# Performance work log

Hardware: AMD Instinct MI355X
Metric: run time of the kernel (lower is better)

The kernel has to match this reference:

```python
import jax, jax.numpy as jnp
import numpy as np

B, T, D, H, DFF = 2, 2048, 1024, 16, 4096
DK = D // H
EPS = 1e-12
NEG = -1e9

def _ln(x, g, b):
    m = jnp.mean(x, axis=-1, keepdims=True)
    v = jnp.mean((x - m) ** 2, axis=-1, keepdims=True)
    return (x - m) / jnp.sqrt(v + EPS) * g + b

def setup_inputs() -> dict:
    key = jax.random.key(0)
    ks = jax.random.split(key, 8)
    s = 0.02
    return {
        "x": jax.random.normal(ks[0], (B, T, D), jnp.float32),
        "mask": jnp.ones((1, 1, T, T), jnp.int32),
        "wq": jax.random.normal(ks[1], (D, D), jnp.float32) * s,
        "bq": jnp.zeros((D,), jnp.float32),
        "wk": jax.random.normal(ks[2], (D, D), jnp.float32) * s,
        "bk": jnp.zeros((D,), jnp.float32),
        "wv": jax.random.normal(ks[3], (D, D), jnp.float32) * s,
        "bv": jnp.zeros((D,), jnp.float32),
        "wo": jax.random.normal(ks[4], (D, D), jnp.float32) * s,
        "bo": jnp.zeros((D,), jnp.float32),
        "w1": jax.random.normal(ks[5], (DFF, D), jnp.float32) * s,
        "b1": jnp.zeros((DFF,), jnp.float32),
        "w2": jax.random.normal(ks[6], (D, DFF), jnp.float32) * s,
        "b2": jnp.zeros((D,), jnp.float32),
        "g1": jnp.ones((D,), jnp.float32),
        "beta1": jnp.zeros((D,), jnp.float32),
        "g2": jnp.ones((D,), jnp.float32),
        "beta2": jnp.zeros((D,), jnp.float32),
    }

def reference(x, mask, wq, bq, wk, bk, wv, bv, wo, bo, w1, b1, w2, b2, g1, beta1, g2, beta2):
    # pre-norm (note: residual taken from ln1 output, faithful to source)
    xn = _ln(x, g1, beta1)
    # torch Linear: y = x @ W.T + b
    def proj(w, b):
        return (jnp.einsum('btd,ed->bte', xn, w) + b).reshape(B, T, H, DK).transpose(0, 2, 1, 3)
    q = proj(wq, bq)  # [B,H,T,DK]
    k = proj(wk, bk)
    v = proj(wv, bv)
    scores = jnp.einsum('bhqd,bhkd->bhqk', q, k) / jnp.sqrt(jnp.float32(DK))
    scores = jnp.where(mask == 0, jnp.float32(NEG), scores)
    weights = jax.nn.softmax(scores, axis=-1)  # dropout is identity in eval
    att = jnp.einsum('bhqk,bhkd->bhqd', weights, v)
    att = att.transpose(0, 2, 1, 3).reshape(B, T, D)
    h = jnp.einsum('btd,ed->bte', att, wo) + bo
    x = xn + h
    x = _ln(x, g2, beta2)
    ff = jax.nn.relu(jnp.einsum('btd,fd->btf', x, w1) + b1)
    ff = jnp.einsum('btf,df->btd', ff, w2) + b2
    return x + ff
```

## Files before the change

### kernel.cpp

```cpp
#include <hip/hip_runtime.h>

typedef unsigned short u16;
typedef __attribute__((ext_vector_type(8))) short short8;
typedef __attribute__((ext_vector_type(4))) float f32x4;
typedef __attribute__((ext_vector_type(4))) unsigned short u16x4;
typedef __attribute__((ext_vector_type(2))) unsigned int u32x2;

#define DEV static __device__ __forceinline__

DEV u16 f2b(float f) {
    unsigned int u = __builtin_bit_cast(unsigned int, f);
    u += 0x7FFFu + ((u >> 16) & 1u);
    return (u16)(u >> 16);
}
DEV float b2f(u16 v) {
    unsigned int u = ((unsigned int)v) << 16;
    return __builtin_bit_cast(float, u);
}
DEV void gload16(const void* g, void* l) {
    __builtin_amdgcn_global_load_lds((const __attribute__((address_space(1))) void*)g,
                                     (__attribute__((address_space(3))) void*)l,
                                     16, 0, 0);
}
DEV unsigned int cvt_pk(float lo, float hi) {
    unsigned int r;
    asm("v_cvt_pk_bf16_f32 %0, %1, %2" : "=v"(r) : "v"(lo), "v"(hi));
    return r;
}

static constexpr float KSCALE = 0.18033688011112042f;

__global__ __launch_bounds__(256) void cvt_all_k(
    const float* __restrict__ wq, const float* __restrict__ wk,
    const float* __restrict__ wv, const float* __restrict__ wo,
    const float* __restrict__ w1, const float* __restrict__ w2,
    u16* __restrict__ wqkv, u16* __restrict__ wo_b,
    u16* __restrict__ w1_b, u16* __restrict__ w2_b) {
    int bid = blockIdx.x;
    const float* s; u16* d; int off;
    if (bid < 1024)      { s = wq; d = wqkv;              off = bid; }
    else if (bid < 2048) { s = wk; d = wqkv + 1024*1024;  off = bid - 1024; }
    else if (bid < 3072) { s = wv; d = wqkv + 2048*1024;  off = bid - 2048; }
    else if (bid < 4096) { s = wo; d = wo_b;              off = bid - 3072; }
    else if (bid < 8192) { s = w1; d = w1_b;              off = bid - 4096; }
    else                 { s = w2; d = w2_b;              off = bid - 8192; }
    int i = off * 256 + threadIdx.x;
    float4 v = ((const float4*)s)[i];
    u16x4 o;
    o[0] = f2b(v.x); o[1] = f2b(v.y); o[2] = f2b(v.z); o[3] = f2b(v.w);
    ((u16x4*)d)[i] = o;
}

template <int INTYPE>
__global__ __launch_bounds__(256) void ln_k(const void* __restrict__ in,
                                            const float* __restrict__ g,
                                            const float* __restrict__ be,
                                            u16* __restrict__ outb) {
    int row = blockIdx.x;
    int t = threadIdx.x;
    float v[4];
    if constexpr (INTYPE == 0) {
        float4 x = ((const float4*)((const float*)in + (size_t)row * 1024))[t];
        v[0] = x.x; v[1] = x.y; v[2] = x.z; v[3] = x.w;
    } else {
        u16x4 x = ((const u16x4*)((const u16*)in + (size_t)row * 1024))[t];
#pragma unroll
        for (int i = 0; i < 4; i++) v[i] = b2f(x[i]);
    }
    float s = v[0] + v[1] + v[2] + v[3];
    float s2 = v[0] * v[0] + v[1] * v[1] + v[2] * v[2] + v[3] * v[3];
#pragma unroll
    for (int off = 1; off < 64; off <<= 1) {
        s += __shfl_xor(s, off);
        s2 += __shfl_xor(s2, off);
    }
    __shared__ float red[8];
    int wid = t >> 6, lane = t & 63;
    if (lane == 0) { red[wid] = s; red[4 + wid] = s2; }
    __syncthreads();
    float S = red[0] + red[1] + red[2] + red[3];
    float S2 = red[4] + red[5] + red[6] + red[7];
    float mean = S * (1.f / 1024.f);
    float var = fmaxf(S2 * (1.f / 1024.f) - mean * mean, 0.f);
    float rinv = rsqrtf(var + 1e-12f);
    float4 gv = ((const float4*)g)[t];
    float4 bv = ((const float4*)be)[t];
    u16x4 o;
    o[0] = f2b((v[0] - mean) * rinv * gv.x + bv.x);
    o[1] = f2b((v[1] - mean) * rinv * gv.y + bv.y);
    o[2] = f2b((v[2] - mean) * rinv * gv.z + bv.z);
    o[3] = f2b((v[3] - mean) * rinv * gv.w + bv.w);
    ((u16x4*)(outb + (size_t)row * 1024))[t] = o;
}

template <int EPI>
__global__ __launch_bounds__(512, 2) void gemm256(
    const u16* __restrict__ A, const u16* __restrict__ Bw,
    const float* __restrict__ b0, const float* __restrict__ b1,
    const float* __restrict__ b2, u16* __restrict__ outb,
    u16* __restrict__ vt, int M, int N, int K) {
    __shared__ u16 SB[3 * 16384];
    int tid = threadIdx.x, wid = tid >> 6, lane = tid & 63;
    int l15 = lane & 15, l4 = lane >> 4;
    int m0 = blockIdx.y * 256, n0 = blockIdx.x * 256;
    int wr = wid >> 2, wc = wid & 3;

    f32x4 acc[8][4] = {};

    int srow = tid >> 2;
    int sc = (tid & 3) * 8;
    const u16* Ag  = A  + (size_t)(m0 + srow) * K + sc;
    const u16* Ag2 = Ag + (size_t)128 * K;
    const u16* Bg  = Bw + (size_t)(n0 + srow) * K + sc;
    const u16* Bg2 = Bg + (size_t)128 * K;
    int ldst = wid * 1024;

    auto stageA = [&](int t, int bufi) {
        char* base = (char*)SB + bufi * 32768;
        size_t ko = (size_t)t * 32;
        gload16(Ag + ko, base + ldst);
        gload16(Ag2 + ko, base + 8192 + ldst);
    };
    auto stageB = [&](int t, int bufi) {
        char* base = (char*)SB + bufi * 32768 + 16384;
        size_t ko = (size_t)t * 32;
        gload16(Bg + ko, base + ldst);
        gload16(Bg2 + ko, base + 8192 + ldst);
    };

    const int NT = K >> 5;
    stageA(0, 0); stageB(0, 0);
    stageA(1, 1); stageB(1, 1);

    int cb = 0;
    for (int i = 0; i < NT; ++i) {
        if (i == NT - 1) asm volatile("s_waitcnt vmcnt(0)" ::: "memory");
        else             asm volatile("s_waitcnt vmcnt(4)" ::: "memory");
        __builtin_amdgcn_s_barrier();
        __builtin_amdgcn_sched_barrier(0);
        int sb = cb + 2; if (sb >= 3) sb -= 3;

        const u16* Abuf = SB + cb * 16384;
        const u16* Bbuf = Abuf + 8192;
        const u16* ap = &Abuf[(wr * 128 + l15) * 32 + l4 * 8];
        const u16* bp = &Bbuf[(wc * 64 + l15) * 32 + l4 * 8];
        short8 af[8], bfr[4];
#pragma unroll
        for (int x = 0; x < 4; x++) {
            af[x]  = *(const short8*)(ap + x * 512);
            bfr[x] = *(const short8*)(bp + x * 512);
        }
        if (i + 2 < NT) stageA(i + 2, sb);
#pragma unroll
        for (int x = 4; x < 8; x++) af[x] = *(const short8*)(ap + x * 512);
        if (i + 2 < NT) stageB(i + 2, sb);
        __builtin_amdgcn_s_setprio(1);
#pragma unroll
        for (int mi = 0; mi < 8; mi++)
#pragma unroll
            for (int ni = 0; ni < 4; ni++)
                acc[mi][ni] = __builtin_amdgcn_mfma_f32_16x16x32_bf16(
                    af[mi], bfr[ni], acc[mi][ni], 0, 0, 0);
        __builtin_amdgcn_s_setprio(0);
        cb = (cb == 2) ? 0 : cb + 1;
    }

#pragma unroll
    for (int mi = 0; mi < 8; mi++) {
#pragma unroll
        for (int ni = 0; ni < 4; ni++) {
            int n = n0 + wc * 64 + ni * 16 + l15;
            int mr = m0 + wr * 128 + mi * 16 + l4 * 4;
            if constexpr (EPI == 0) {
                if (n0 < 2048) {
                    float bias = (n < 1024) ? b0[n] : b1[n - 1024];
                    float scale = (n < 1024) ? 1.f : KSCALE;
#pragma unroll
                    for (int r = 0; r < 4; r++)
                        outb[(size_t)(mr + r) * 2048 + n] =
                            f2b((acc[mi][ni][r] + bias) * scale);
                } else {
                    float bias = b2[n - 2048];
                    int bidx = m0 >> 11;
                    int tb = mr & 2047;
                    u16x4 pk;
#pragma unroll
                    for (int r = 0; r < 4; r++) pk[r] = f2b(acc[mi][ni][r] + bias);
                    *(u16x4*)&vt[((size_t)(bidx * 1024 + (n - 2048))) * 2048 + tb] = pk;
                }
            } else {
                float bias = b0[n];
#pragma unroll
                for (int r = 0; r < 4; r++)
                    outb[(size_t)(mr + r) * N + n] =
                        f2b(fmaxf(acc[mi][ni][r] + bias, 0.f));
            }
        }
    }
}

template <int EPI, int BM>
__global__ __launch_bounds__(256) void gemm_bt(
    const u16* __restrict__ A, const u16* __restrict__ Bw,
    const float* __restrict__ b0, u16* __restrict__ outb,
    float* __restrict__ outf, const u16* __restrict__ res,
    int M, int N, int K) {
    constexpr int MFR = BM / 32;
    constexpr int BS = (BM + 128) * 32;
    __shared__ u16 SB[3 * BS];
    int tid = threadIdx.x, wid = tid >> 6, lane = tid & 63;
    int l15 = lane & 15, l4 = lane >> 4;
    int m0 = blockIdx.y * BM, n0 = blockIdx.x * 128;
    int wr = wid >> 1, wc = wid & 1;

    f32x4 acc[MFR][4] = {};

    int srow = tid >> 2;
    int scol = (tid & 3) * 8;
    const u16* Ag  = A  + (size_t)(m0 + srow) * K + scol;
    const u16* Ag2 = Ag + (size_t)64 * K;
    const u16* Bg  = Bw + (size_t)(n0 + srow) * K + scol;
    const u16* Bg2 = Bg + (size_t)64 * K;
    int ldst = wid * 1024;

    auto stage = [&](int t, int bufi) {
        char* base = (char*)SB + (size_t)bufi * (BS * 2);
        size_t ko = (size_t)t * 32;
        gload16(Ag + ko, base + ldst);
        if constexpr (BM == 128) gload16(Ag2 + ko, base + 4096 + ldst);
        gload16(Bg + ko, base + BM * 64 + ldst);
        gload16(Bg2 + ko, base + BM * 64 + 4096 + ldst);
    };

    const int NT = K >> 5;
    stage(0, 0);
    stage(1, 1);

    int cb = 0;
    for (int i = 0; i < NT; ++i) {
        if (i == NT - 1) {
            asm volatile("s_waitcnt vmcnt(0)" ::: "memory");
        } else if constexpr (BM == 128) {
            asm volatile("s_waitcnt vmcnt(4)" ::: "memory");
        } else {
            asm volatile("s_waitcnt vmcnt(3)" ::: "memory");
        }
        __builtin_amdgcn_s_barrier();
        __builtin_amdgcn_sched_barrier(0);
        int sb = cb + 2; if (sb >= 3) sb -= 3;
        if (i + 2 < NT) stage(i + 2, sb);

        const u16* Abuf = SB + (size_t)cb * BS;
        const u16* Bbuf = Abuf + BM * 32;
        short8 af[MFR], bfr[4];
        const u16* ap = &Abuf[(wr * (BM / 2) + l15) * 32 + l4 * 8];
        const u16* bp = &Bbuf[(wc * 64 + l15) * 32 + l4 * 8];
#pragma unroll
        for (int i2 = 0; i2 < MFR; i2++) af[i2] = *(const short8*)(ap + i2 * 512);
#pragma unroll
        for (int i2 = 0; i2 < 4; i2++) bfr[i2] = *(const short8*)(bp + i2 * 512);
#pragma unroll
        for (int mi = 0; mi < MFR; mi++)
#pragma unroll
            for (int ni = 0; ni < 4; ni++)
                acc[mi][ni] = __builtin_amdgcn_mfma_f32_16x16x32_bf16(
                    af[mi], bfr[ni], acc[mi][ni], 0, 0, 0);
        cb = (cb == 2) ? 0 : cb + 1;
    }

    int mbase = m0 + wr * (BM / 2);
    int nbase = n0 + wc * 64;
#pragma unroll
    for (int mi = 0; mi < MFR; mi++) {
#pragma unroll
        for (int ni = 0; ni < 4; ni++) {
            int n = nbase + ni * 16 + l15;
            int mr = mbase + mi * 16 + l4 * 4;
            float bias = b0[n];
            if constexpr (EPI == 1) {
#pragma unroll
                for (int i = 0; i < 4; i++) {
                    size_t off = (size_t)(mr + i) * N + n;
                    outb[off] = f2b(acc[mi][ni][i] + bias + b2f(res[off]));
                }
            } else {
#pragma unroll
                for (int i = 0; i < 4; i++) {
                    size_t off = (size_t)(mr + i) * N + n;
                    outf[off] = acc[mi][ni][i] + bias + b2f(res[off]);
                }
            }
        }
    }
}

#define ATT_STAGE(KN, VN, TILE) do {                                          \
    size_t koff_ = (size_t)(TILE) * 64 * 2048;                                \
    gload16(Kg + koff_, (char*)(KN) + ldst);                                  \
    gload16(Kg + koff_ + 32 * 2048, (char*)(KN) + 4096 + ldst);               \
    gload16(Vg + (TILE) * 64, (char*)(VN) + ldst);                            \
    gload16(Vg + (TILE) * 64 + 32 * 2048, (char*)(VN) + 4096 + ldst);         \
} while (0)

#define ATT_BODY(KL, VL, PRE, WAITSTR) do {                                   \
    PRE;                                                                      \
    asm volatile("s_waitcnt " WAITSTR ::: "memory");                          \
    __builtin_amdgcn_s_barrier();                                             \
    __builtin_amdgcn_sched_barrier(0);                                        \
    f32x4 s_acc[4][2] = {};                                                   \
    _Pragma("unroll")                                                         \
    for (int kvt = 0; kvt < 4; kvt++) {                                       \
        int row = kvt * 16 + l15;                                             \
        short8 kf0 = *(const short8*)&(KL)[row * 64 + ((l4) ^ (row & 7)) * 8]; \
        short8 kf1 = *(const short8*)&(KL)[row * 64 + ((4 + l4) ^ (row & 7)) * 8]; \
        _Pragma("unroll")                                                     \
        for (int qfi = 0; qfi < 2; qfi++) {                                   \
            s_acc[kvt][qfi] = __builtin_amdgcn_mfma_f32_16x16x32_bf16(        \
                kf0, qf[qfi][0], s_acc[kvt][qfi], 0, 0, 0);                   \
            s_acc[kvt][qfi] = __builtin_amdgcn_mfma_f32_16x16x32_bf16(        \
                kf1, qf[qfi][1], s_acc[kvt][qfi], 0, 0, 0);                   \
        }                                                                     \
    }                                                                         \
    _Pragma("unroll")                                                         \
    for (int qfi = 0; qfi < 2; qfi++) {                                       \
        char* Pq = Pw + qfi * 2176;                                           \
        _Pragma("unroll")                                                     \
        for (int kvt = 0; kvt < 4; kvt++) {                                   \
            u32x2 w;                                                          \
            w[0] = cvt_pk(exp2f(s_acc[kvt][qfi][0]), exp2f(s_acc[kvt][qfi][1])); \
            w[1] = cvt_pk(exp2f(s_acc[kvt][qfi][2]), exp2f(s_acc[kvt][qfi][3])); \
            *(u32x2*)(Pq + l15 * 136 + kvt * 32 + l4 * 8) = w;                \
        }                                                                     \
    }                                                                         \
    {                                                                         \
        short8 pf[2][2];                                                      \
        _Pragma("unroll")                                                     \
        for (int qfi = 0; qfi < 2; qfi++) {                                   \
            char* Pq = Pw + qfi * 2176;                                       \
            pf[qfi][0] = *(const short8*)(Pq + l15 * 136 + l4 * 16);          \
            pf[qfi][1] = *(const short8*)(Pq + l15 * 136 + 64 + l4 * 16);     \
            o_sum[qfi] = __builtin_amdgcn_mfma_f32_16x16x32_bf16(             \
                ones, pf[qfi][0], o_sum[qfi], 0, 0, 0);                       \
            o_sum[qfi] = __builtin_amdgcn_mfma_f32_16x16x32_bf16(             \
                ones, pf[qfi][1], o_sum[qfi], 0, 0, 0);                       \
        }                                                                     \
        _Pragma("unroll")                                                     \
        for (int dt = 0; dt < 4; dt++) {                                      \
            int row = dt * 16 + l15;                                          \
            short8 vf0 = *(const short8*)&(VL)[row * 64 + ((l4) ^ (row & 7)) * 8]; \
            short8 vf1 = *(const short8*)&(VL)[row * 64 + ((4 + l4) ^ (row & 7)) * 8]; \
            _Pragma("unroll")                                                 \
            for (int qfi = 0; qfi < 2; qfi++) {                               \
                o_acc[dt][qfi] = __builtin_amdgcn_mfma_f32_16x16x32_bf16(     \
                    vf0, pf[qfi][0], o_acc[dt][qfi], 0, 0, 0);                \
                o_acc[dt][qfi] = __builtin_amdgcn_mfma_f32_16x16x32_bf16(     \
                    vf1, pf[qfi][1], o_acc[dt][qfi], 0, 0, 0);                \
            }                                                                 \
        }                                                                     \
    }                                                                         \
    __builtin_amdgcn_sched_barrier(0);                                        \
    __builtin_amdgcn_s_barrier();                                             \
} while (0)

__global__ __launch_bounds__(256, 2) void attn_k(const u16* __restrict__ qk,
                                                 const u16* __restrict__ vt,
                                                 u16* __restrict__ att) {
    __shared__ u16 K_lds[2][64 * 64];
    __shared__ u16 V_lds[2][64 * 64];
    __shared__ u16 P_lds[4][2][16 * 68];
    int tid = threadIdx.x, wid = tid >> 6, lane = tid & 63;
    int l15 = lane & 15, l4 = lane >> 4;
    int bh = blockIdx.y, b = bh >> 4, h = bh & 15;
    size_t boff = (size_t)b * 2048;
    size_t hoff = (size_t)b * 1024 + h * 64;
    int q0 = blockIdx.x * 128 + wid * 32;

    short8 qf[2][2];
#pragma unroll
    for (int qfi = 0; qfi < 2; qfi++) {
        const u16* qb = qk + (boff + q0 + qfi * 16 + l15) * 2048 + h * 64 + l4 * 8;
        qf[qfi][0] = *(const short8*)(qb);
        qf[qfi][1] = *(const short8*)(qb + 32);
    }
    short8 ones;
#pragma unroll
    for (int j = 0; j < 8; j++) ones[j] = (short)0x3F80;

    f32x4 o_acc[4][2] = {};
    f32x4 o_sum[2] = {};
    char* Pw = (char*)&P_lds[wid][0][0];

    int srow = tid >> 3, scs = (tid & 7) ^ (srow & 7);
    const u16* Kg = qk + (boff + srow) * 2048 + 1024 + h * 64 + scs * 8;
    const u16* Vg = vt + (hoff + srow) * 2048 + scs * 8;
    int ldst = wid * 1024;

    ATT_STAGE(&K_lds[0][0], &V_lds[0][0], 0);
    for (int kt2 = 0; kt2 < 15; kt2++) {
        ATT_BODY(&K_lds[0][0], &V_lds[0][0],
                 ATT_STAGE(&K_lds[1][0], &V_lds[1][0], 2 * kt2 + 1), "vmcnt(4)");
        ATT_BODY(&K_lds[1][0], &V_lds[1][0],
                 ATT_STAGE(&K_lds[0][0], &V_lds[0][0], 2 * kt2 + 2), "vmcnt(4)");
    }
    ATT_BODY(&K_lds[0][0], &V_lds[0][0],
             ATT_STAGE(&K_lds[1][0], &V_lds[1][0], 31), "vmcnt(4)");
    ATT_BODY(&K_lds[1][0], &V_lds[1][0], ((void)0), "vmcnt(0)");

#pragma unroll
    for (int qfi = 0; qfi < 2; qfi++) {
        float rl = 1.f / o_sum[qfi][0];
#pragma unroll
        for (int dt = 0; dt < 4; dt++) {
            u16x4 o;
#pragma unroll
            for (int r = 0; r < 4; r++) o[r] = f2b(o_acc[dt][qfi][r] * rl);
            *(u16x4*)&att[(boff + q0 + qfi * 16 + l15) * 1024 + h * 64 +
                          dt * 16 + l4 * 4] = o;
        }
    }
}

extern "C" void kernel_launch(void* const* d_in, const int* in_sizes, int n_in,
                              void* d_out, int out_size, void* d_ws, size_t ws_size,
                              hipStream_t stream) {
    (void)in_sizes; (void)n_in; (void)out_size; (void)ws_size;
    const float* x   = (const float*)d_in[0];
    const float* wq  = (const float*)d_in[2];
    const float* bq  = (const float*)d_in[3];
    const float* wk  = (const float*)d_in[4];
    const float* bk  = (const float*)d_in[5];
    const float* wv  = (const float*)d_in[6];
    const float* bv  = (const float*)d_in[7];
    const float* wo  = (const float*)d_in[8];
    const float* bo  = (const float*)d_in[9];
    const float* w1  = (const float*)d_in[10];
    const float* b1  = (const float*)d_in[11];
    const float* w2  = (const float*)d_in[12];
    const float* b2  = (const float*)d_in[13];
    const float* g1  = (const float*)d_in[14];
    const float* be1 = (const float*)d_in[15];
    const float* g2  = (const float*)d_in[16];
    const float* be2 = (const float*)d_in[17];
    float* out = (float*)d_out;

    char* ws = (char*)d_ws;
    u16* wqkv  = (u16*)(ws + (size_t)0);
    u16* wo_b  = (u16*)(ws + ((size_t)6  << 20));
    u16* w1_b  = (u16*)(ws + ((size_t)8  << 20));
    u16* w2_b  = (u16*)(ws + ((size_t)16 << 20));
    u16* xn_b  = (u16*)(ws + ((size_t)24 << 20));
    u16* x2_b  = (u16*)(ws + ((size_t)32 << 20));
    u16* x3_b  = (u16*)(ws + ((size_t)40 << 20));
    u16* qk_b  = (u16*)(ws + ((size_t)48 << 20));
    u16* vt_b  = (u16*)(ws + ((size_t)64 << 20));
    u16* att_b = (u16*)(ws + ((size_t)72 << 20));
    u16* ff_b  = (u16*)(ws + ((size_t)48 << 20));

    cvt_all_k<<<12288, 256, 0, stream>>>(wq, wk, wv, wo, w1, w2,
                                         wqkv, wo_b, w1_b, w2_b);
    ln_k<0><<<4096, 256, 0, stream>>>(x, g1, be1, xn_b);
    gemm256<0><<<dim3(12, 16), 512, 0, stream>>>(
        xn_b, wqkv, bq, bk, bv, qk_b, vt_b, 4096, 3072, 1024);
    attn_k<<<dim3(16, 32), 256, 0, stream>>>(qk_b, vt_b, att_b);
    gemm_bt<1, 64><<<dim3(8, 64), 256, 0, stream>>>(
        att_b, wo_b, bo, x2_b, nullptr, xn_b, 4096, 1024, 1024);
    ln_k<1><<<4096, 256, 0, stream>>>(x2_b, g2, be2, x3_b);
    gemm256<2><<<dim3(16, 16), 512, 0, stream>>>(
        x3_b, w1_b, b1, nullptr, nullptr, ff_b, nullptr, 4096, 4096, 1024);
    gemm_bt<3, 64><<<dim3(8, 64), 256, 0, stream>>>(
        ff_b, w2_b, b2, nullptr, out, x3_b, 4096, 1024, 4096);
}
```

Baseline: 255.5 us.

## Split attention over key halves and add a combine kernel

The attention kernel now splits the 2048 keys into two halves using a third grid dimension, doubling the block count. Each half writes unnormalized bf16 partial outputs and per-row softmax sums into workspace buffers. A new combine kernel adds the two partials and divides by the summed denominators. Launch bounds are raised to request three blocks per CU. The aim is better CU occupancy and latency hiding, at the cost of an extra kernel launch, extra global traffic and rounding of unnormalized partials to bf16.

```diff
diff --git a/kernel.cpp b/kernel.cpp
--- a/kernel.cpp
+++ b/kernel.cpp
@@ -362,15 +362,19 @@
     __builtin_amdgcn_s_barrier();                                             \
 } while (0)
 
-__global__ __launch_bounds__(256, 2) void attn_k(const u16* __restrict__ qk,
+__global__ __launch_bounds__(256, 3) void attn_k(const u16* __restrict__ qk,
                                                  const u16* __restrict__ vt,
-                                                 u16* __restrict__ att) {
+                                                 u16* __restrict__ p0,
+                                                 u16* __restrict__ p1,
+                                                 float* __restrict__ s0,
+                                                 float* __restrict__ s1) {
     __shared__ u16 K_lds[2][64 * 64];
     __shared__ u16 V_lds[2][64 * 64];
     __shared__ u16 P_lds[4][2][16 * 68];
     int tid = threadIdx.x, wid = tid >> 6, lane = tid & 63;
     int l15 = lane & 15, l4 = lane >> 4;
     int bh = blockIdx.y, b = bh >> 4, h = bh & 15;
+    int z = blockIdx.z;
     size_t boff = (size_t)b * 2048;
     size_t hoff = (size_t)b * 1024 + h * 64;
     int q0 = blockIdx.x * 128 + wid * 32;
@@ -391,33 +395,58 @@
     char* Pw = (char*)&P_lds[wid][0][0];
 
     int srow = tid >> 3, scs = (tid & 7) ^ (srow & 7);
-    const u16* Kg = qk + (boff + srow) * 2048 + 1024 + h * 64 + scs * 8;
-    const u16* Vg = vt + (hoff + srow) * 2048 + scs * 8;
+    const u16* Kg = qk + (boff + z * 1024 + srow) * 2048 + 1024 + h * 64 + scs * 8;
+    const u16* Vg = vt + (hoff + srow) * 2048 + z * 1024 + scs * 8;
     int ldst = wid * 1024;
 
     ATT_STAGE(&K_lds[0][0], &V_lds[0][0], 0);
-    for (int kt2 = 0; kt2 < 15; kt2++) {
+    for (int kt2 = 0; kt2 < 7; kt2++) {
         ATT_BODY(&K_lds[0][0], &V_lds[0][0],
                  ATT_STAGE(&K_lds[1][0], &V_lds[1][0], 2 * kt2 + 1), "vmcnt(4)");
         ATT_BODY(&K_lds[1][0], &V_lds[1][0],
                  ATT_STAGE(&K_lds[0][0], &V_lds[0][0], 2 * kt2 + 2), "vmcnt(4)");
     }
     ATT_BODY(&K_lds[0][0], &V_lds[0][0],
-             ATT_STAGE(&K_lds[1][0], &V_lds[1][0], 31), "vmcnt(4)");
+             ATT_STAGE(&K_lds[1][0], &V_lds[1][0], 15), "vmcnt(4)");
     ATT_BODY(&K_lds[1][0], &V_lds[1][0], ((void)0), "vmcnt(0)");
 
+    u16* pz = z ? p1 : p0;
+    float* sz = z ? s1 : s0;
 #pragma unroll
     for (int qfi = 0; qfi < 2; qfi++) {
-        float rl = 1.f / o_sum[qfi][0];
+        int q = q0 + qfi * 16 + l15;
 #pragma unroll
         for (int dt = 0; dt < 4; dt++) {
             u16x4 o;
 #pragma unroll
-            for (int r = 0; r < 4; r++) o[r] = f2b(o_acc[dt][qfi][r] * rl);
-            *(u16x4*)&att[(boff + q0 + qfi * 16 + l15) * 1024 + h * 64 +
-                          dt * 16 + l4 * 4] = o;
+            for (int r = 0; r < 4; r++) o[r] = f2b(o_acc[dt][qfi][r]);
+            *(u16x4*)&pz[(boff + q) * 1024 + h * 64 + dt * 16 + l4 * 4] = o;
         }
-    }
+        if (l4 == 0) sz[(boff + q) * 16 + h] = o_sum[qfi][0];
+    }
+}
+
+__global__ __launch_bounds__(256) void attn_cmb(
+    const u16* __restrict__ p0, const u16* __restrict__ p1,
+    const float* __restrict__ s0, const float* __restrict__ s1,
+    u16* __restrict__ att) {
+    int idx = blockIdx.x * 256 + threadIdx.x;
+    int row = idx >> 7, oct = idx & 127;
+    int h = oct >> 3;
+    float rs = 1.f / (s0[row * 16 + h] + s1[row * 16 + h]);
+    size_t off = (size_t)row * 1024 + oct * 8;
+    u16x4 a0 = ((const u16x4*)(p0 + off))[0];
+    u16x4 a1 = ((const u16x4*)(p0 + off))[1];
+    u16x4 c0 = ((const u16x4*)(p1 + off))[0];
+    u16x4 c1 = ((const u16x4*)(p1 + off))[1];
+    u16x4 o0, o1;
+#pragma unroll
+    for (int j = 0; j < 4; j++) {
+        o0[j] = f2b((b2f(a0[j]) + b2f(c0[j])) * rs);
+        o1[j] = f2b((b2f(a1[j]) + b2f(c1[j])) * rs);
+    }
+    ((u16x4*)(att + off))[0] = o0;
+    ((u16x4*)(att + off))[1] = o1;
 }
 
 extern "C" void kernel_launch(void* const* d_in, const int* in_sizes, int n_in,
@@ -454,6 +483,8 @@
     u16* qk_b  = (u16*)(ws + ((size_t)48 << 20));
     u16* vt_b  = (u16*)(ws + ((size_t)64 << 20));
     u16* att_b = (u16*)(ws + ((size_t)72 << 20));
+    float* s0_b = (float*)(ws + ((size_t)80 << 20));
+    float* s1_b = (float*)(ws + ((size_t)80 << 20) + 262144);
     u16* ff_b  = (u16*)(ws + ((size_t)48 << 20));
 
     cvt_all_k<<<12288, 256, 0, stream>>>(wq, wk, wv, wo, w1, w2,
@@ -461,7 +492,9 @@
     ln_k<0><<<4096, 256, 0, stream>>>(x, g1, be1, xn_b);
     gemm256<0><<<dim3(12, 16), 512, 0, stream>>>(
         xn_b, wqkv, bq, bk, bv, qk_b, vt_b, 4096, 3072, 1024);
-    attn_k<<<dim3(16, 32), 256, 0, stream>>>(qk_b, vt_b, att_b);
+    attn_k<<<dim3(16, 32, 2), 256, 0, stream>>>(qk_b, vt_b, x2_b, x3_b,
+                                                s0_b, s1_b);
+    attn_cmb<<<2048, 256, 0, stream>>>(x2_b, x3_b, s0_b, s1_b, att_b);
     gemm_bt<1, 64><<<dim3(8, 64), 256, 0, stream>>>(
         att_b, wo_b, bo, x2_b, nullptr, xn_b, 4096, 1024, 1024);
     ln_k<1><<<4096, 256, 0, stream>>>(x2_b, g2, be2, x3_b);
```

Measured after the change: 257.4 us. About the same (+0.7%).
